# Kernel tuning notes

Hardware: AMD Instinct MI355X
Metric: run time of the kernel (lower is better)

## Reference

```python
import jax, jax.numpy as jnp
import numpy as np

B, C, H, W = 2, 64, 512, 512
HEADS = 4
EPS = 1e-12  # F.normalize eps


def setup_inputs() -> dict:
    key = jax.random.key(0)
    ks = jax.random.split(key, 7)
    s = 0.02
    return {
        "x": jax.random.normal(ks[0], (B, C, H, W), jnp.float32),
        "Wq": jax.random.normal(ks[1], (C, C), jnp.float32) * s,
        "Wk": jax.random.normal(ks[2], (C, C), jnp.float32) * s,
        "Wv": jax.random.normal(ks[3], (C, C), jnp.float32) * s,
        "Wp": jax.random.normal(ks[4], (C, C), jnp.float32) * s,
        "bp": jax.random.normal(ks[5], (C,), jnp.float32) * s,
        "rescale": jnp.ones((HEADS, 1, 1), jnp.float32),
    }


def reference(x, Wq, Wk, Wv, Wp, bp, rescale):
    b, c, h, w = x.shape
    n = h * w
    d = c // HEADS
    xf = x.reshape(b, c, n)  # 1x1 conv == channel matmul on flattened spatial

    def conv1x1(Wt):
        return jnp.einsum('oc,bcn->bon', Wt, xf)

    # torch: permute->reshape(b,n,c)->split heads->transpose == reshape conv out to (b,heads,d,n)
    q = conv1x1(Wq).reshape(b, HEADS, d, n)
    k = conv1x1(Wk).reshape(b, HEADS, d, n)
    v = conv1x1(Wv).reshape(b, HEADS, d, n)

    def l2norm(t):  # F.normalize(p=2, dim=-1)
        nrm = jnp.sqrt(jnp.sum(t * t, axis=-1, keepdims=True))
        return t / jnp.maximum(nrm, EPS)

    q = l2norm(q)
    k = l2norm(k)

    attn = jnp.einsum('bhdn,bhen->bhde', k, q)  # (b, heads, d, d) tiny matrix
    attn = attn * rescale  # rescale broadcasts (heads,1,1)
    attn = jax.nn.softmax(attn, axis=-1)

    o = jnp.einsum('bhde,bhen->bhdn', attn, v).reshape(b, c, n)
    out = jnp.einsum('oc,bcn->bon', Wp, o) + bp[None, :, None] + xf  # proj + residual
    return out.reshape(b, c, h, w)
```

## Files before the change

### kernel.cpp

```cpp
#include <hip/hip_runtime.h>
#include <math.h>

#define C 64
#define NHEADS 4
#define DH 16
#define NN 262144
#define NB 2
#define PB 512
#define NT 2
#define EPS 1e-12f

typedef __attribute__((ext_vector_type(8))) short short8v;
typedef __attribute__((ext_vector_type(8))) unsigned short ushort8v;
typedef __attribute__((ext_vector_type(4))) float f32x4;

static __device__ __forceinline__ unsigned short f2bf(float f) {
  union { float f; unsigned int u; } v; v.f = f;
  unsigned int r = v.u + 0x7fffu + ((v.u >> 16) & 1u);
  return (unsigned short)(r >> 16);
}

__global__ __launch_bounds__(256, 2) void gram_kernel(const float* __restrict__ x,
                                                      float* __restrict__ Gc) {
  __shared__ unsigned short xs[C * 256];
  const int b = blockIdx.y;
  const int chunk = blockIdx.x;
  const float* xb = x + (size_t)b * C * NN;
  const int t = threadIdx.x;
  const int w = t >> 6, l = t & 63;
  const int lrow = l & 15, lhi = l >> 4;

  const int gA0 = (w >> 1) * 2, gA1 = gA0 + 1;
  const int gB0 = (w & 1) * 2,  gB1 = gB0 + 1;
  const int cA0 = gA0 * 16 + lrow, cA1 = gA1 * 16 + lrow;
  const int cB0 = gB0 * 16 + lrow, cB1 = gB1 * 16 + lrow;

  f32x4 acc0 = {0.f,0.f,0.f,0.f}, acc1 = {0.f,0.f,0.f,0.f};
  f32x4 acc2 = {0.f,0.f,0.f,0.f}, acc3 = {0.f,0.f,0.f,0.f};

  for (int tile = 0; tile < NT; ++tile) {
    const int j0 = (chunk * NT + tile) * 256;
    __syncthreads();
#pragma unroll
    for (int i = 0; i < 8; ++i) {
      const int oi = i * 256 + t;
      const int c = oi >> 5, oct = oi & 31;
      const float* src = xb + (size_t)c * NN + j0 + oct * 8;
      const float4 v0 = *reinterpret_cast<const float4*>(src);
      const float4 v1 = *reinterpret_cast<const float4*>(src + 4);
      ushort8v pk;
      pk[0] = f2bf(v0.x); pk[1] = f2bf(v0.y); pk[2] = f2bf(v0.z); pk[3] = f2bf(v0.w);
      pk[4] = f2bf(v1.x); pk[5] = f2bf(v1.y); pk[6] = f2bf(v1.z); pk[7] = f2bf(v1.w);
      *reinterpret_cast<ushort8v*>(&xs[c * 256 + ((oct ^ (c & 7)) << 3)]) = pk;
    }
    __syncthreads();
#pragma unroll
    for (int s = 0; s < 8; ++s) {
      const int o = s * 4 + lhi;
      const short8v fA0 = *reinterpret_cast<const short8v*>(&xs[cA0 * 256 + ((o ^ (cA0 & 7)) << 3)]);
      const short8v fA1 = *reinterpret_cast<const short8v*>(&xs[cA1 * 256 + ((o ^ (cA1 & 7)) << 3)]);
      const short8v fB0 = *reinterpret_cast<const short8v*>(&xs[cB0 * 256 + ((o ^ (cB0 & 7)) << 3)]);
      const short8v fB1 = *reinterpret_cast<const short8v*>(&xs[cB1 * 256 + ((o ^ (cB1 & 7)) << 3)]);
      acc0 = __builtin_amdgcn_mfma_f32_16x16x32_bf16(fA0, fB0, acc0, 0, 0, 0);
      acc1 = __builtin_amdgcn_mfma_f32_16x16x32_bf16(fA0, fB1, acc1, 0, 0, 0);
      acc2 = __builtin_amdgcn_mfma_f32_16x16x32_bf16(fA1, fB0, acc2, 0, 0, 0);
      acc3 = __builtin_amdgcn_mfma_f32_16x16x32_bf16(fA1, fB1, acc3, 0, 0, 0);
    }
  }
  float* g = Gc + ((size_t)b * PB + chunk) * 4096;
#pragma unroll
  for (int r = 0; r < 4; ++r) {
    const int row = lhi * 4 + r;
    g[(gA0 * 16 + row) * 64 + gB0 * 16 + lrow] = acc0[r];
    g[(gA0 * 16 + row) * 64 + gB1 * 16 + lrow] = acc1[r];
    g[(gA1 * 16 + row) * 64 + gB0 * 16 + lrow] = acc2[r];
    g[(gA1 * 16 + row) * 64 + gB1 * 16 + lrow] = acc3[r];
  }
}

__global__ __launch_bounds__(256) void reduce_kernel(const float* __restrict__ Gc,
                                                     float* __restrict__ G) {
  __shared__ float s[4][64];
  const int b = blockIdx.y;
  const int g = blockIdx.x;
  const int t = threadIdx.x;
  const int e = g * 64 + (t & 63);
  const int chunk = t >> 6;
  float sum = 0.f;
  for (int p = chunk; p < PB; p += 4)
    sum += Gc[((size_t)b * PB + p) * 4096 + e];
  s[chunk][t & 63] = sum;
  __syncthreads();
  if (t < 64) G[(size_t)b * 4096 + g * 64 + t] = s[0][t] + s[1][t] + s[2][t] + s[3][t];
}

__global__ __launch_bounds__(256) void attn_kernel(const float* __restrict__ G,
    const float* __restrict__ Wq, const float* __restrict__ Wk,
    const float* __restrict__ Wv, const float* __restrict__ Wp,
    const float* __restrict__ rescale, float* __restrict__ E) {
  __shared__ float Gs[4096], GQt[4096], GKt[4096], T[4096];
  __shared__ float attnw[64][DH];
  __shared__ float nq[64], nk[64];
  const int b = blockIdx.x;
  const int t = threadIdx.x;

  for (int i = t; i < 4096; i += 256) Gs[i] = G[(size_t)b * 4096 + i];
  __syncthreads();
  for (int i = t; i < 4096; i += 256) {
    const int c = i >> 6, e = i & 63;
    float sq_ = 0.f, sk_ = 0.f;
    for (int c2 = 0; c2 < 64; ++c2) {
      const float g = Gs[c * 64 + c2];
      sq_ += g * Wq[e * 64 + c2];
      sk_ += g * Wk[e * 64 + c2];
    }
    GQt[c * 64 + e] = sq_;
    GKt[c * 64 + e] = sk_;
  }
  __syncthreads();
  if (t < 64) {
    float s = 0.f;
    for (int c2 = 0; c2 < 64; ++c2) s += Wq[t * 64 + c2] * GQt[c2 * 64 + t];
    nq[t] = sqrtf(fmaxf(s, 0.f));
  } else if (t < 128) {
    const int d = t - 64;
    float s = 0.f;
    for (int c2 = 0; c2 < 64; ++c2) s += Wk[d * 64 + c2] * GKt[c2 * 64 + d];
    nk[d] = sqrtf(fmaxf(s, 0.f));
  }
  __syncthreads();
  if (t < 64) {
    const int h = t >> 4;
    const float rs = rescale[h];
    const float nkd = fmaxf(nk[t], EPS);
    float logits[DH];
    float mx = -1e30f;
    for (int ee = 0; ee < DH; ++ee) {
      const int e = h * DH + ee;
      float num = 0.f;
      for (int c2 = 0; c2 < 64; ++c2) num += Wk[t * 64 + c2] * GQt[c2 * 64 + e];
      const float l = num / (nkd * fmaxf(nq[e], EPS)) * rs;
      logits[ee] = l;
      mx = fmaxf(mx, l);
    }
    float sum = 0.f;
    for (int ee = 0; ee < DH; ++ee) { const float p = expf(logits[ee] - mx); logits[ee] = p; sum += p; }
    const float inv = 1.f / sum;
    for (int ee = 0; ee < DH; ++ee) attnw[t][ee] = logits[ee] * inv;
  }
  __syncthreads();
  for (int i = t; i < 4096; i += 256) {
    const int r = i >> 6, c = i & 63;
    const int h = r >> 4;
    float s = 0.f;
    for (int e = 0; e < DH; ++e) s += attnw[r][e] * Wv[(h * DH + e) * 64 + c];
    T[i] = s;
  }
  __syncthreads();
  for (int i = t; i < 4096; i += 256) {
    const int r = i >> 6, c = i & 63;
    float s = (r == c) ? 1.f : 0.f;
    for (int m = 0; m < 64; ++m) s += Wp[r * 64 + m] * T[m * 64 + c];
    E[(size_t)b * 4096 + i] = s;
  }
}

__global__ __launch_bounds__(256, 2) void apply_kernel(const float* __restrict__ x,
    const float* __restrict__ E, const float* __restrict__ bp,
    float* __restrict__ out) {
  __shared__ float xt[C * 128];
  __shared__ float Mt[C * 68];
  const int blk = blockIdx.x;
  const int b = blk >> 9;
  const int chunk = blk & 511;
  const float* xb = x + (size_t)b * C * NN;
  float* ob = out + (size_t)b * C * NN;
  const int t = threadIdx.x;
  const int wid = t >> 6, lane = t & 63;
  const int ly = lane >> 3, lx = lane & 7;

  for (int i = t; i < 4096; i += 256) {
    const int k = i >> 6, c = i & 63;
    Mt[k * 68 + c] = E[(size_t)b * 4096 + c * 64 + k];
  }

  for (int tile = 0; tile < 4; ++tile) {
    const int j0 = chunk * 512 + tile * 128;
    __syncthreads();
#pragma unroll
    for (int i = 0; i < 8; ++i) {
      const int idx = i * 256 + t;
      const int c = idx >> 5, jq = idx & 31;
      const float4 v = *reinterpret_cast<const float4*>(xb + (size_t)c * NN + j0 + jq * 4);
      const int sq = jq ^ ((c >> 3) & 7);
      *reinterpret_cast<float4*>(&xt[c * 128 + sq * 4]) = v;
    }
    __syncthreads();
    const int qL = wid * 8 + lx;
    float acc[8][4];
#pragma unroll
    for (int a = 0; a < 8; ++a)
#pragma unroll
      for (int r = 0; r < 4; ++r) acc[a][r] = 0.f;
#pragma unroll 4
    for (int k = 0; k < 64; ++k) {
      const float4 m0 = *reinterpret_cast<const float4*>(&Mt[k * 68 + ly * 8]);
      const float4 m1 = *reinterpret_cast<const float4*>(&Mt[k * 68 + ly * 8 + 4]);
      const float4 xv = *reinterpret_cast<const float4*>(&xt[k * 128 + ((qL ^ ((k >> 3) & 7)) << 2)]);
      const float mv[8] = {m0.x, m0.y, m0.z, m0.w, m1.x, m1.y, m1.z, m1.w};
#pragma unroll
      for (int a = 0; a < 8; ++a) {
        acc[a][0] += mv[a] * xv.x;
        acc[a][1] += mv[a] * xv.y;
        acc[a][2] += mv[a] * xv.z;
        acc[a][3] += mv[a] * xv.w;
      }
    }
#pragma unroll
    for (int a = 0; a < 8; ++a) {
      const int c1 = ly * 8 + a;
      const float bias = bp[c1];
      float4 o4;
      o4.x = acc[a][0] + bias;
      o4.y = acc[a][1] + bias;
      o4.z = acc[a][2] + bias;
      o4.w = acc[a][3] + bias;
      *reinterpret_cast<float4*>(&ob[(size_t)c1 * NN + j0 + qL * 4]) = o4;
    }
  }
}

extern "C" void kernel_launch(void* const* d_in, const int* in_sizes, int n_in,
                              void* d_out, int out_size, void* d_ws, size_t ws_size,
                              hipStream_t stream) {
  const float* x       = (const float*)d_in[0];
  const float* Wq      = (const float*)d_in[1];
  const float* Wk      = (const float*)d_in[2];
  const float* Wv      = (const float*)d_in[3];
  const float* Wp      = (const float*)d_in[4];
  const float* bp      = (const float*)d_in[5];
  const float* rescale = (const float*)d_in[6];
  float* out = (float*)d_out;

  float* Gc = out;
  float* G  = (float*)d_ws;
  float* E  = G + (size_t)NB * 4096;

  gram_kernel<<<dim3(PB, NB), dim3(256), 0, stream>>>(x, Gc);
  reduce_kernel<<<dim3(64, NB), dim3(256), 0, stream>>>(Gc, G);
  attn_kernel<<<dim3(NB), dim3(256), 0, stream>>>(G, Wq, Wk, Wv, Wp, rescale, E);
  apply_kernel<<<dim3(1024), dim3(256), 0, stream>>>(x, E, bp, out);
}
```

Before: 181.6 us.

## Run apply stage on bf16 MFMA with bf16 combined matrix and smaller tiles

Rewrites the final apply kernel to convert x tiles to bf16 in swizzled shared memory and compute E·x with 16x16x32 bf16 MFMA instructions instead of fp32 FMA loops. The attention kernel now stores the combined projection matrix E in bf16, and the grid is retiled to 128-column blocks with higher occupancy bounds. The aim is to cut ALU time in the apply pass, at the cost of bf16 rounding on the residual path (identity folded into E) and scalar rather than vectorized output stores.

```diff
diff --git a/kernel.cpp b/kernel.cpp
--- a/kernel.cpp
+++ b/kernel.cpp
@@ -12,6 +12,7 @@
 
 typedef __attribute__((ext_vector_type(8))) short short8v;
 typedef __attribute__((ext_vector_type(8))) unsigned short ushort8v;
+typedef __attribute__((ext_vector_type(4))) unsigned short ushort4v;
 typedef __attribute__((ext_vector_type(4))) float f32x4;
 
 static __device__ __forceinline__ unsigned short f2bf(float f) {
@@ -97,7 +98,7 @@
 __global__ __launch_bounds__(256) void attn_kernel(const float* __restrict__ G,
     const float* __restrict__ Wq, const float* __restrict__ Wk,
     const float* __restrict__ Wv, const float* __restrict__ Wp,
-    const float* __restrict__ rescale, float* __restrict__ E) {
+    const float* __restrict__ rescale, unsigned short* __restrict__ Ebf) {
   __shared__ float Gs[4096], GQt[4096], GKt[4096], T[4096];
   __shared__ float attnw[64][DH];
   __shared__ float nq[64], nk[64];
@@ -161,71 +162,80 @@
     const int r = i >> 6, c = i & 63;
     float s = (r == c) ? 1.f : 0.f;
     for (int m = 0; m < 64; ++m) s += Wp[r * 64 + m] * T[m * 64 + c];
-    E[(size_t)b * 4096 + i] = s;
-  }
-}
-
-__global__ __launch_bounds__(256, 2) void apply_kernel(const float* __restrict__ x,
-    const float* __restrict__ E, const float* __restrict__ bp,
+    Ebf[(size_t)b * 4096 + i] = f2bf(s);
+  }
+}
+
+__global__ __launch_bounds__(256, 4) void apply_kernel(const float* __restrict__ x,
+    const unsigned short* __restrict__ Ebf, const float* __restrict__ bp,
     float* __restrict__ out) {
-  __shared__ float xt[C * 128];
-  __shared__ float Mt[C * 68];
-  const int blk = blockIdx.x;
-  const int b = blk >> 9;
-  const int chunk = blk & 511;
+  __shared__ unsigned short xt[128 * 64];
+  const int b = blockIdx.y;
+  const int n0 = blockIdx.x * 128;
   const float* xb = x + (size_t)b * C * NN;
   float* ob = out + (size_t)b * C * NN;
   const int t = threadIdx.x;
-  const int wid = t >> 6, lane = t & 63;
-  const int ly = lane >> 3, lx = lane & 7;
-
-  for (int i = t; i < 4096; i += 256) {
-    const int k = i >> 6, c = i & 63;
-    Mt[k * 68 + c] = E[(size_t)b * 4096 + c * 64 + k];
-  }
-
-  for (int tile = 0; tile < 4; ++tile) {
-    const int j0 = chunk * 512 + tile * 128;
-    __syncthreads();
-#pragma unroll
-    for (int i = 0; i < 8; ++i) {
-      const int idx = i * 256 + t;
-      const int c = idx >> 5, jq = idx & 31;
-      const float4 v = *reinterpret_cast<const float4*>(xb + (size_t)c * NN + j0 + jq * 4);
-      const int sq = jq ^ ((c >> 3) & 7);
-      *reinterpret_cast<float4*>(&xt[c * 128 + sq * 4]) = v;
-    }
-    __syncthreads();
-    const int qL = wid * 8 + lx;
-    float acc[8][4];
-#pragma unroll
-    for (int a = 0; a < 8; ++a)
-#pragma unroll
-      for (int r = 0; r < 4; ++r) acc[a][r] = 0.f;
-#pragma unroll 4
-    for (int k = 0; k < 64; ++k) {
-      const float4 m0 = *reinterpret_cast<const float4*>(&Mt[k * 68 + ly * 8]);
-      const float4 m1 = *reinterpret_cast<const float4*>(&Mt[k * 68 + ly * 8 + 4]);
-      const float4 xv = *reinterpret_cast<const float4*>(&xt[k * 128 + ((qL ^ ((k >> 3) & 7)) << 2)]);
-      const float mv[8] = {m0.x, m0.y, m0.z, m0.w, m1.x, m1.y, m1.z, m1.w};
-#pragma unroll
-      for (int a = 0; a < 8; ++a) {
-        acc[a][0] += mv[a] * xv.x;
-        acc[a][1] += mv[a] * xv.y;
-        acc[a][2] += mv[a] * xv.z;
-        acc[a][3] += mv[a] * xv.w;
+  const int w = t >> 6, l = t & 63;
+  const int lrow = l & 15, lhi = l >> 4;
+
+  short8v ef[4][2];
+  const unsigned short* eb = Ebf + (size_t)b * 4096;
+#pragma unroll
+  for (int ot = 0; ot < 4; ++ot)
+#pragma unroll
+    for (int ks = 0; ks < 2; ++ks)
+      ef[ot][ks] = *reinterpret_cast<const short8v*>(eb + (ot * 16 + lrow) * 64 + ks * 32 + lhi * 8);
+
+#pragma unroll
+  for (int h = 0; h < 2; ++h) {
+    const int n = h * 64 + l;
+#pragma unroll
+    for (int i = 0; i < 4; ++i) {
+      const int c0 = w * 16 + i * 4;
+      const float v0 = xb[(size_t)(c0 + 0) * NN + n0 + n];
+      const float v1 = xb[(size_t)(c0 + 1) * NN + n0 + n];
+      const float v2 = xb[(size_t)(c0 + 2) * NN + n0 + n];
+      const float v3 = xb[(size_t)(c0 + 3) * NN + n0 + n];
+      ushort4v pk;
+      pk[0] = f2bf(v0); pk[1] = f2bf(v1); pk[2] = f2bf(v2); pk[3] = f2bf(v3);
+      const int q = c0 >> 2;
+      *reinterpret_cast<ushort4v*>(
+          &xt[n * 64 + ((((q >> 1) ^ (n & 7)) << 3) + (q & 1) * 4)]) = pk;
+    }
+  }
+  __syncthreads();
+
+  f32x4 acc[4][2];
+#pragma unroll
+  for (int ot = 0; ot < 4; ++ot)
+#pragma unroll
+    for (int nn = 0; nn < 2; ++nn) acc[ot][nn] = (f32x4){0.f, 0.f, 0.f, 0.f};
+
+  const int nbase = w * 32;
+#pragma unroll
+  for (int nn = 0; nn < 2; ++nn) {
+    const int n = nbase + nn * 16 + lrow;
+#pragma unroll
+    for (int ks = 0; ks < 2; ++ks) {
+      const int s = ks * 4 + lhi;
+      const short8v xf = *reinterpret_cast<const short8v*>(&xt[n * 64 + ((s ^ (n & 7)) << 3)]);
+#pragma unroll
+      for (int ot = 0; ot < 4; ++ot)
+        acc[ot][nn] = __builtin_amdgcn_mfma_f32_16x16x32_bf16(ef[ot][ks], xf, acc[ot][nn], 0, 0, 0);
+    }
+  }
+
+#pragma unroll
+  for (int ot = 0; ot < 4; ++ot) {
+#pragma unroll
+    for (int r = 0; r < 4; ++r) {
+      const int o = ot * 16 + lhi * 4 + r;
+      const float bias = bp[o];
+#pragma unroll
+      for (int nn = 0; nn < 2; ++nn) {
+        const int n = nbase + nn * 16 + lrow;
+        ob[(size_t)o * NN + n0 + n] = acc[ot][nn][r] + bias;
       }
-    }
-#pragma unroll
-    for (int a = 0; a < 8; ++a) {
-      const int c1 = ly * 8 + a;
-      const float bias = bp[c1];
-      float4 o4;
-      o4.x = acc[a][0] + bias;
-      o4.y = acc[a][1] + bias;
-      o4.z = acc[a][2] + bias;
-      o4.w = acc[a][3] + bias;
-      *reinterpret_cast<float4*>(&ob[(size_t)c1 * NN + j0 + qL * 4]) = o4;
     }
   }
 }
@@ -244,10 +254,10 @@
 
   float* Gc = out;
   float* G  = (float*)d_ws;
-  float* E  = G + (size_t)NB * 4096;
+  unsigned short* Ebf = (unsigned short*)(G + (size_t)NB * 4096);
 
   gram_kernel<<<dim3(PB, NB), dim3(256), 0, stream>>>(x, Gc);
   reduce_kernel<<<dim3(64, NB), dim3(256), 0, stream>>>(Gc, G);
-  attn_kernel<<<dim3(NB), dim3(256), 0, stream>>>(G, Wq, Wk, Wv, Wp, rescale, E);
-  apply_kernel<<<dim3(1024), dim3(256), 0, stream>>>(x, E, bp, out);
-}
+  attn_kernel<<<dim3(NB), dim3(256), 0, stream>>>(G, Wq, Wk, Wv, Wp, rescale, Ebf);
+  apply_kernel<<<dim3(2048, NB), dim3(256), 0, stream>>>(x, Ebf, bp, out);
+}
```

Measured after the change: 155.7 us. -14.2%, faster.
